# Kernel tuning notes

Measured on AMD Instinct MI355X. Metric: run time of the kernel, lower is better.

The kernel has to match this reference:

```python
import jax, jax.numpy as jnp
import numpy as np

B, N, NFEAT, NHID = 64, 133, 75, 128


def _uniform(key, shape, stdv):
    return jax.random.uniform(key, shape, minval=-stdv, maxval=stdv, dtype=jnp.float32)


def setup_inputs() -> dict:
    key = jax.random.key(0)
    ks = jax.random.split(key, 20)
    x = jax.random.normal(ks[0], (B, N, NFEAT), dtype=jnp.float32)
    mask = jax.random.uniform(ks[1], (B, N, N)) < 0.08
    adj = jnp.where(mask, jax.random.uniform(ks[2], (B, N, N), dtype=jnp.float32), 0.0)

    def lin(k, fin, fout):  # torch Linear default init ~ U(-1/sqrt(fin), 1/sqrt(fin))
        s = 1.0 / np.sqrt(fin)
        k1, k2 = jax.random.split(k)
        return _uniform(k1, (fin, fout), s), _uniform(k2, (fout,), s)

    def gc(k, fin, fout):  # GraphConvolution init ~ U(-1/sqrt(fout), 1/sqrt(fout))
        s = 1.0 / np.sqrt(fout)
        k1, k2 = jax.random.split(k)
        return _uniform(k1, (fin, fout), s), _uniform(k2, (fout,), s)

    emb_w, emb_b = lin(ks[3], NFEAT, 2 * NFEAT)
    gc1_w, gc1_b = gc(ks[4], 2 * NFEAT, 2 * NHID)
    gc2_w, gc2_b = gc(ks[5], 2 * NHID, NHID)
    gc3_w, gc3_b = gc(ks[6], NHID, NFEAT)
    gc4_w, gc4_b = gc(ks[7], NFEAT, 1)
    fc1_w, fc1_b = lin(ks[8], N - 1, 3)
    fin_w, fin_b = lin(ks[9], 4, 1)
    return dict(x=x, adj=adj, emb_w=emb_w, emb_b=emb_b,
                gc1_w=gc1_w, gc1_b=gc1_b, gc2_w=gc2_w, gc2_b=gc2_b,
                gc3_w=gc3_w, gc3_b=gc3_b, gc4_w=gc4_w, gc4_b=gc4_b,
                fc1_w=fc1_w, fc1_b=fc1_b, fin_w=fin_w, fin_b=fin_b)


def _gcn(x, adj, w, b):
    # output = adj @ (x @ W) + b   for each batch element
    return jnp.einsum('bij,bjf->bif', adj, x @ w) + b


def _graph_pooling(x, neibs):
    # per node i: max over features of neighbors j with neibs[b,i,j]; 0 if no neighbors
    masked = jnp.where(neibs[:, :, :, None], x[:, None, :, :], -jnp.inf)  # [B,N,N,F]
    pooled = jnp.max(masked, axis=2)                                       # [B,N,F]
    has_nb = jnp.any(neibs, axis=2)[:, :, None]                            # [B,N,1]
    return jnp.where(has_nb, pooled, 0.0)


def reference(x, adj, emb_w, emb_b, gc1_w, gc1_b, gc2_w, gc2_b,
              gc3_w, gc3_b, gc4_w, gc4_b, fc1_w, fc1_b, fin_w, fin_b):
    neibs = adj > 1e-5                                   # [B,N,N] bool
    h = jax.nn.relu(x @ emb_w + emb_b)                   # [B,N,2*nfeat]
    h = jax.nn.relu(_gcn(h, adj, gc1_w, gc1_b))          # [B,N,2*nhid]
    h = _graph_pooling(h, neibs)
    h = jax.nn.relu(_gcn(h, adj, gc2_w, gc2_b))          # [B,N,nhid]
    h = _graph_pooling(h, neibs)
    h = jax.nn.relu(_gcn(h, adj, gc3_w, gc3_b))          # [B,N,nfeat]
    h = _graph_pooling(h, neibs)
    h = jax.nn.relu(_gcn(h, adj, gc4_w, gc4_b))          # [B,N,1]
    h = h.reshape(h.shape[0], 1, -1)                     # [B,1,N]
    fst = h[:, :, :1]                                    # [B,1,1]
    rest = h[:, :, 1:]                                   # [B,1,N-1]
    # dropout is identity in eval mode
    rest = rest @ fc1_w + fc1_b                          # [B,1,3]
    out = jnp.concatenate((fst, rest), axis=2)           # [B,1,4]
    return jax.nn.sigmoid(out @ fin_w + fin_b)           # [B,1,1]
```

## Files before the change

kernel.cpp:

```cpp
#include <hip/hip_runtime.h>
#include <math.h>


#define NN 133
#define NPAIR 64
#define NW 16
#define ST 264

typedef float v4f __attribute__((ext_vector_type(4)));
typedef _Float16 f16x8 __attribute__((ext_vector_type(8)));
typedef _Float16 f16x4 __attribute__((ext_vector_type(4)));
typedef float f32x4 __attribute__((ext_vector_type(4)));

#define WP_EMB 0
#define WP_GC1 15360
#define WP_GC2 56320
#define WP_GC3 89088
#define WP_TOT 99328

struct Params {
    const float *x, *adj, *emb_w, *emb_b, *gc1_w, *gc1_b, *gc2_w, *gc2_b,
                *gc3_w, *gc3_b, *gc4_w, *gc4_b, *fc1_w, *fc1_b, *fin_w, *fin_b;
    const _Float16 *wp;
    float2 *gpairs;
    float *out;
};

__global__ __launch_bounds__(64)
void wpack_k(const float* __restrict__ emb_w, const float* __restrict__ gc1_w,
             const float* __restrict__ gc2_w, const float* __restrict__ gc3_w,
             _Float16* __restrict__ wp)
{
    const int t = blockIdx.x, lane = threadIdx.x;
    const float* W; int K, N, NKS, off, u;
    if (t < 30)       { W = emb_w; K = 75;  N = 150; NKS = 3; off = WP_EMB; u = t; }
    else if (t < 110) { W = gc1_w; K = 150; N = 256; NKS = 5; off = WP_GC1; u = t - 30; }
    else if (t < 174) { W = gc2_w; K = 256; N = 128; NKS = 8; off = WP_GC2; u = t - 110; }
    else              { W = gc3_w; K = 128; N = 75;  NKS = 4; off = WP_GC3; u = t - 174; }
    const int ct = u / NKS, ks = u % NKS;
    const int col = ct * 16 + (lane & 15);
    const int kb  = ks * 32 + (lane >> 4) * 8;
    f16x8 v;
#pragma unroll
    for (int j = 0; j < 8; ++j) {
        const int kk = kb + j;
        float w = W[(size_t)min(kk, K - 1) * N + min(col, N - 1)];
        if (kk >= K || col >= N) w = 0.f;
        v[j] = (_Float16)w;
    }
    *reinterpret_cast<f16x8*>(wp + (size_t)off + (size_t)u * 512 + lane * 8) = v;
}

__device__ __forceinline__ void prep_row_g(
    const float* __restrict__ ar, float2* __restrict__ pb,
    int2* __restrict__ cS, int r, int lane)
{
    const unsigned long long lt = (1ull << lane) - 1ull;
    int base0 = 0, base1 = 0;
#pragma unroll
    for (int s = 0; s < 3; ++s) {
        const int j = lane + 64 * s;
        const float a = (j < NN) ? ar[j] : 0.f;
        const bool f = a > 1e-5f;
        const bool g = (a > 0.f) && !f;
        const unsigned long long mf = __ballot(f);
        const unsigned long long mg = __ballot(g);
        if (f) pb[base0 + __popcll(mf & lt)] =
                   make_float2(a, __int_as_float(j));
        if (g) pb[(NPAIR - 1) - (base1 + __popcll(mg & lt))] =
                   make_float2(a, __int_as_float(j));
        base0 += __popcll(mf);
        base1 += __popcll(mg);
    }
    if (lane == 0) cS[r] = make_int2(base0, base1);
}

template<int KPAD, int N, int STN, int NTC, bool RB>
__device__ __forceinline__ void mfma_gemm(
    const _Float16* __restrict__ Af, const _Float16* __restrict__ Wp,
    const float* __restrict__ bias, _Float16* __restrict__ outl,
    int wave, int lane)
{
    const int lrow = lane & 15, lkb = lane >> 4;
    for (int t = wave; t < NTC * 9; t += NW) {
        const int ct = t % NTC, rt = t / NTC;
        const int col = ct * 16 + lrow;
        const _Float16* ap  = Af + (rt * 16 + lrow) * ST + lkb * 8;
        const _Float16* wpt = Wp + (size_t)(ct * (KPAD / 32)) * 512 + lane * 8;
        f32x4 acc = {0.f, 0.f, 0.f, 0.f};
#pragma unroll
        for (int ks = 0; ks < KPAD / 32; ++ks) {
            f16x8 a  = *reinterpret_cast<const f16x8*>(ap + ks * 32);
            f16x8 bf = *reinterpret_cast<const f16x8*>(wpt + ks * 512);
            acc = __builtin_amdgcn_mfma_f32_16x16x32_f16(a, bf, acc, 0, 0, 0);
        }
#pragma unroll
        for (int i = 0; i < 4; ++i) {
            const int row = rt * 16 + lkb * 4 + i;
            if (row < NN && col < STN) {
                float v = 0.f;
                if (col < N) {
                    v = acc[i];
                    if (RB) v = fmaxf(v + bias[col], 0.f);
                }
                outl[row * ST + col] = (_Float16)v;
            }
        }
    }
}

__device__ __forceinline__ void spmm4_lds(
    const _Float16* __restrict__ tb, const float* __restrict__ bias,
    const float2* __restrict__ pb, int2 cc,
    _Float16* __restrict__ yrow, int lane)
{
    const int c0 = 4 * lane;
    const float4* pq = reinterpret_cast<const float4*>(pb);
    float a0[4] = {}, a1[4] = {}, a2[4] = {}, a3[4] = {};
    int q = 0;
    for (; q + 4 <= cc.x; q += 4) {
        float4 p0 = pq[q >> 1], p1 = pq[(q >> 1) + 1];
        f16x4 r0 = *(const f16x4*)(tb + __float_as_int(p0.y) * ST + c0);
        f16x4 r1 = *(const f16x4*)(tb + __float_as_int(p0.w) * ST + c0);
        f16x4 r2 = *(const f16x4*)(tb + __float_as_int(p1.y) * ST + c0);
        f16x4 r3 = *(const f16x4*)(tb + __float_as_int(p1.w) * ST + c0);
#pragma unroll
        for (int u = 0; u < 4; ++u) {
            a0[u] = fmaf(p0.x, (float)r0[u], a0[u]);
            a1[u] = fmaf(p0.z, (float)r1[u], a1[u]);
            a2[u] = fmaf(p1.x, (float)r2[u], a2[u]);
            a3[u] = fmaf(p1.z, (float)r3[u], a3[u]);
        }
    }
    for (; q < cc.x; ++q) {
        float2 f = pb[q];
        f16x4 r = *(const f16x4*)(tb + __float_as_int(f.y) * ST + c0);
#pragma unroll
        for (int u = 0; u < 4; ++u) a0[u] = fmaf(f.x, (float)r[u], a0[u]);
    }
    for (int v = 0; v < cc.y; ++v) {
        float2 f = pb[(NPAIR - 1) - v];
        f16x4 r = *(const f16x4*)(tb + __float_as_int(f.y) * ST + c0);
#pragma unroll
        for (int u = 0; u < 4; ++u) a0[u] = fmaf(f.x, (float)r[u], a0[u]);
    }
    f16x4 o;
#pragma unroll
    for (int u = 0; u < 4; ++u) {
        float s = (a0[u] + a1[u]) + (a2[u] + a3[u]);
        o[u] = (_Float16)fmaxf(s + bias[c0 + u], 0.f);
    }
    *(f16x4*)(yrow + c0) = o;
}

__device__ __forceinline__ void pool4_lds(
    const _Float16* __restrict__ yb,
    const float2* __restrict__ pb, int cx,
    _Float16* __restrict__ prow, int lane)
{
    const int c0 = 4 * lane;
    const float4* pq = reinterpret_cast<const float4*>(pb);
    float m0[4] = {}, m1[4] = {}, m2[4] = {}, m3[4] = {};
    int q = 0;
    for (; q + 4 <= cx; q += 4) {
        float4 p0 = pq[q >> 1], p1 = pq[(q >> 1) + 1];
        f16x4 r0 = *(const f16x4*)(yb + __float_as_int(p0.y) * ST + c0);
        f16x4 r1 = *(const f16x4*)(yb + __float_as_int(p0.w) * ST + c0);
        f16x4 r2 = *(const f16x4*)(yb + __float_as_int(p1.y) * ST + c0);
        f16x4 r3 = *(const f16x4*)(yb + __float_as_int(p1.w) * ST + c0);
#pragma unroll
        for (int u = 0; u < 4; ++u) {
            m0[u] = fmaxf(m0[u], (float)r0[u]);
            m1[u] = fmaxf(m1[u], (float)r1[u]);
            m2[u] = fmaxf(m2[u], (float)r2[u]);
            m3[u] = fmaxf(m3[u], (float)r3[u]);
        }
    }
    for (; q < cx; ++q) {
        f16x4 r = *(const f16x4*)(yb + __float_as_int(pb[q].y) * ST + c0);
#pragma unroll
        for (int u = 0; u < 4; ++u) m0[u] = fmaxf(m0[u], (float)r[u]);
    }
    f16x4 o;
#pragma unroll
    for (int u = 0; u < 4; ++u)
        o[u] = (_Float16)fmaxf(fmaxf(m0[u], m1[u]), fmaxf(m2[u], m3[u]));
    *(f16x4*)(prow + c0) = o;
}

__device__ __forceinline__ void spmm2_lds(
    const _Float16* __restrict__ tb, const float* __restrict__ bias, int N,
    const float2* __restrict__ pb, int2 cc,
    _Float16* __restrict__ yrow, int lane)
{
    const int c0 = 2 * lane;
    const float4* pq = reinterpret_cast<const float4*>(pb);
    float a0[2] = {}, a1[2] = {}, a2[2] = {}, a3[2] = {};
    int q = 0;
    for (; q + 4 <= cc.x; q += 4) {
        float4 p0 = pq[q >> 1], p1 = pq[(q >> 1) + 1];
        f16x4 rr0 = *(const f16x4*)nullptr, rr1;
        (void)rr0; (void)rr1;
        const _Float16* t0 = tb + __float_as_int(p0.y) * ST + c0;
        const _Float16* t1 = tb + __float_as_int(p0.w) * ST + c0;
        const _Float16* t2 = tb + __float_as_int(p1.y) * ST + c0;
        const _Float16* t3 = tb + __float_as_int(p1.w) * ST + c0;
#pragma unroll
        for (int u = 0; u < 2; ++u) {
            a0[u] = fmaf(p0.x, (float)t0[u], a0[u]);
            a1[u] = fmaf(p0.z, (float)t1[u], a1[u]);
            a2[u] = fmaf(p1.x, (float)t2[u], a2[u]);
            a3[u] = fmaf(p1.z, (float)t3[u], a3[u]);
        }
    }
    for (; q < cc.x; ++q) {
        float2 f = pb[q];
        const _Float16* t0 = tb + __float_as_int(f.y) * ST + c0;
#pragma unroll
        for (int u = 0; u < 2; ++u) a0[u] = fmaf(f.x, (float)t0[u], a0[u]);
    }
    for (int v = 0; v < cc.y; ++v) {
        float2 f = pb[(NPAIR - 1) - v];
        const _Float16* t0 = tb + __float_as_int(f.y) * ST + c0;
#pragma unroll
        for (int u = 0; u < 2; ++u) a0[u] = fmaf(f.x, (float)t0[u], a0[u]);
    }
    float s0 = (a0[0] + a1[0]) + (a2[0] + a3[0]);
    float s1 = (a0[1] + a1[1]) + (a2[1] + a3[1]);
    s0 = fmaxf(s0 + bias[min(c0, N - 1)], 0.f);
    s1 = fmaxf(s1 + bias[min(c0 + 1, N - 1)], 0.f);
    if (c0 + 1 < N) {
        yrow[c0] = (_Float16)s0; yrow[c0 + 1] = (_Float16)s1;
    } else if (c0 < N) {
        yrow[c0] = (_Float16)s0;
    }
}

__device__ __forceinline__ void pool2_lds(
    const _Float16* __restrict__ yb, int N,
    const float2* __restrict__ pb, int cx,
    _Float16* __restrict__ prow, int lane)
{
    const int c0 = 2 * lane;
    const float4* pq = reinterpret_cast<const float4*>(pb);
    float m0[2] = {}, m1[2] = {}, m2[2] = {}, m3[2] = {};
    int q = 0;
    for (; q + 4 <= cx; q += 4) {
        float4 p0 = pq[q >> 1], p1 = pq[(q >> 1) + 1];
        const _Float16* t0 = yb + __float_as_int(p0.y) * ST + c0;
        const _Float16* t1 = yb + __float_as_int(p0.w) * ST + c0;
        const _Float16* t2 = yb + __float_as_int(p1.y) * ST + c0;
        const _Float16* t3 = yb + __float_as_int(p1.w) * ST + c0;
#pragma unroll
        for (int u = 0; u < 2; ++u) {
            m0[u] = fmaxf(m0[u], (float)t0[u]);
            m1[u] = fmaxf(m1[u], (float)t1[u]);
            m2[u] = fmaxf(m2[u], (float)t2[u]);
            m3[u] = fmaxf(m3[u], (float)t3[u]);
        }
    }
    for (; q < cx; ++q) {
        const _Float16* t0 = yb + __float_as_int(pb[q].y) * ST + c0;
#pragma unroll
        for (int u = 0; u < 2; ++u) m0[u] = fmaxf(m0[u], (float)t0[u]);
    }
    if (c0 + 1 < N) {
        prow[c0]     = (_Float16)fmaxf(fmaxf(m0[0], m1[0]), fmaxf(m2[0], m3[0]));
        prow[c0 + 1] = (_Float16)fmaxf(fmaxf(m0[1], m1[1]), fmaxf(m2[1], m3[1]));
    } else if (c0 < N) {
        prow[c0]     = (_Float16)fmaxf(fmaxf(m0[0], m1[0]), fmaxf(m2[0], m3[0]));
    }
}

__device__ __forceinline__ void t4_row_h(
    const _Float16* __restrict__ yb,
    const float2* __restrict__ pb, int cx,
    const float* __restrict__ gc4_w,
    float* __restrict__ t4S, int r, int lane)
{
    const float4* pq = reinterpret_cast<const float4*>(pb);
    const float gw0 = gc4_w[lane];
    const float gw1 = (lane < 11) ? gc4_w[64 + lane] : 0.f;
    const int c2 = 64 + min(lane, 10);

    float m0a = 0.f, m1a = 0.f, m0b = 0.f, m1b = 0.f;
    float m0c = 0.f, m1c = 0.f, m0d = 0.f, m1d = 0.f;
    int q = 0;
    for (; q + 4 <= cx; q += 4) {
        float4 pA = pq[q >> 1], pB = pq[(q >> 1) + 1];
        const _Float16* r0 = yb + __float_as_int(pA.y) * ST;
        const _Float16* r1 = yb + __float_as_int(pA.w) * ST;
        const _Float16* r2 = yb + __float_as_int(pB.y) * ST;
        const _Float16* r3 = yb + __float_as_int(pB.w) * ST;
        m0a = fmaxf(m0a, (float)r0[lane]); m1a = fmaxf(m1a, (float)r0[c2]);
        m0b = fmaxf(m0b, (float)r1[lane]); m1b = fmaxf(m1b, (float)r1[c2]);
        m0c = fmaxf(m0c, (float)r2[lane]); m1c = fmaxf(m1c, (float)r2[c2]);
        m0d = fmaxf(m0d, (float)r3[lane]); m1d = fmaxf(m1d, (float)r3[c2]);
    }
    for (; q < cx; ++q) {
        const _Float16* r0 = yb + __float_as_int(pb[q].y) * ST;
        m0a = fmaxf(m0a, (float)r0[lane]); m1a = fmaxf(m1a, (float)r0[c2]);
    }
    float m0 = fmaxf(fmaxf(m0a, m0b), fmaxf(m0c, m0d));
    float m1 = fmaxf(fmaxf(m1a, m1b), fmaxf(m1c, m1d));
    float v = m0 * gw0 + m1 * gw1;
#pragma unroll
    for (int off = 32; off; off >>= 1) v += __shfl_xor(v, off, 64);
    if (lane == 0) t4S[r] = v;
}

__global__ __launch_bounds__(1024, 1)
void graph_k(Params P)
{
    __shared__ __align__(16) _Float16 BUF[2][144 * ST];
    __shared__ int2  cS[NN];
    __shared__ float t4S[NN];
    __shared__ float y4S[NN];
    __shared__ float rS[3];

    const int b    = blockIdx.x;
    const int tid  = threadIdx.x;
    const int wave = tid >> 6, lane = tid & 63;

    _Float16* B0 = BUF[0];
    _Float16* B1 = BUF[1];
    float2* gp = P.gpairs + (size_t)b * NN * NPAIR;

    {
        v4f* z = reinterpret_cast<v4f*>(&BUF[0][0]);
        for (int i = tid; i < 2 * 144 * ST / 8; i += 1024)
            z[i] = v4f{0.f, 0.f, 0.f, 0.f};
    }
    __syncthreads();
    for (int i = tid; i < NN * 75; i += 1024) {
        int r = i / 75, c = i - r * 75;
        B1[r * ST + c] = (_Float16)P.x[(size_t)b * NN * 75 + i];
    }
    for (int r = wave; r < NN; r += NW)
        prep_row_g(P.adj + ((size_t)b * NN + r) * NN, gp + (size_t)r * NPAIR,
                   cS, r, lane);
    __syncthreads();
    mfma_gemm<96, 150, 150, 10, true>(B1, P.wp + WP_EMB, P.emb_b, B0, wave, lane);
    __syncthreads();
    mfma_gemm<160, 256, 256, 16, false>(B0, P.wp + WP_GC1, nullptr, B1, wave, lane);
    __syncthreads();
    for (int r = wave; r < NN; r += NW)
        spmm4_lds(B1, P.gc1_b, gp + (size_t)r * NPAIR, cS[r],
                  B0 + r * ST, lane);
    __syncthreads();
    for (int r = wave; r < NN; r += NW)
        pool4_lds(B0, gp + (size_t)r * NPAIR, cS[r].x, B1 + r * ST, lane);
    __syncthreads();
    mfma_gemm<256, 128, 128, 8, false>(B1, P.wp + WP_GC2, nullptr, B0, wave, lane);
    __syncthreads();
    for (int r = wave; r < NN; r += NW)
        spmm2_lds(B0, P.gc2_b, 128, gp + (size_t)r * NPAIR, cS[r],
                  B1 + r * ST, lane);
    __syncthreads();
    for (int r = wave; r < NN; r += NW)
        pool2_lds(B1, 128, gp + (size_t)r * NPAIR, cS[r].x, B0 + r * ST, lane);
    __syncthreads();
    mfma_gemm<128, 75, 76, 5, false>(B0, P.wp + WP_GC3, nullptr, B1, wave, lane);
    __syncthreads();
    for (int r = wave; r < NN; r += NW)
        spmm2_lds(B1, P.gc3_b, 75, gp + (size_t)r * NPAIR, cS[r],
                  B0 + r * ST, lane);
    __syncthreads();
    for (int r = wave; r < NN; r += NW)
        t4_row_h(B0, gp + (size_t)r * NPAIR, cS[r].x, P.gc4_w, t4S, r, lane);
    __syncthreads();
    if (tid < NN) {
        const float2* pb = gp + (size_t)tid * NPAIR;
        int2 c = cS[tid];
        float s = P.gc4_b[0];
        for (int q = 0; q < c.x; ++q) {
            float2 f = pb[q];
            s = fmaf(f.x, t4S[__float_as_int(f.y)], s);
        }
        for (int q = 0; q < c.y; ++q) {
            float2 f = pb[(NPAIR - 1) - q];
            s = fmaf(f.x, t4S[__float_as_int(f.y)], s);
        }
        y4S[tid] = fmaxf(s, 0.f);
    }
    __syncthreads();
    if (tid < 3) {
        float s = P.fc1_b[tid];
        for (int j = 0; j < 132; ++j)
            s = fmaf(y4S[1 + j], P.fc1_w[j * 3 + tid], s);
        rS[tid] = s;
    }
    __syncthreads();
    if (tid == 0) {
        float z = P.fin_b[0] + y4S[0] * P.fin_w[0] + rS[0] * P.fin_w[1]
                + rS[1] * P.fin_w[2] + rS[2] * P.fin_w[3];
        P.out[b] = 1.f / (1.f + expf(-z));
    }
}

extern "C" void kernel_launch(void* const* d_in, const int* in_sizes, int n_in,
                              void* d_out, int out_size, void* d_ws, size_t ws_size,
                              hipStream_t stream)
{
    _Float16* wp = (_Float16*)d_ws;
    float2* gpairs = (float2*)((char*)d_ws + (256 << 10));

    Params hp;
    hp.x     = (const float*)d_in[0];
    hp.adj   = (const float*)d_in[1];
    hp.emb_w = (const float*)d_in[2];
    hp.emb_b = (const float*)d_in[3];
    hp.gc1_w = (const float*)d_in[4];
    hp.gc1_b = (const float*)d_in[5];
    hp.gc2_w = (const float*)d_in[6];
    hp.gc2_b = (const float*)d_in[7];
    hp.gc3_w = (const float*)d_in[8];
    hp.gc3_b = (const float*)d_in[9];
    hp.gc4_w = (const float*)d_in[10];
    hp.gc4_b = (const float*)d_in[11];
    hp.fc1_w = (const float*)d_in[12];
    hp.fc1_b = (const float*)d_in[13];
    hp.fin_w = (const float*)d_in[14];
    hp.fin_b = (const float*)d_in[15];
    hp.wp = wp;
    hp.gpairs = gpairs;
    hp.out = (float*)d_out;

    hipLaunchKernelGGL(wpack_k, dim3(194), dim3(64), 0, stream,
                       hp.emb_w, hp.gc1_w, hp.gc2_w, hp.gc3_w, wp);
    hipLaunchKernelGGL(graph_k, dim3(64), dim3(1024), 0, stream, hp);
}
```

Baseline: 188.6 us.

## Replace gather-based sparse aggregation with dense fp16 MFMA adjacency matmul

The pack kernel now also converts each batch's adjacency into fp16 MFMA fragment layout. The graph kernel replaces the per-row gather SpMM loops with dense MFMA GEMMs against that packed adjacency, computing transposed (column-major) feature tiles so adj@T fits the MFMA operand layout. LDS is reorganised into two regions with tighter per-stage strides, and the pooling helpers are adjusted to match. The aim is to put aggregation on the matrix cores instead of scalar FMA gathers. The cost is dense work on a ~8%-sparse matrix, an extra 64 pack blocks that read all of adj, and fp16 rounding of adjacency values.

New measurement: 222.8 us, median of 2. 18.1% more time.

```diff
diff --git a/kernel.cpp b/kernel.cpp
--- a/kernel.cpp
+++ b/kernel.cpp
@@ -5,50 +5,73 @@
 #define NN 133
 #define NPAIR 64
 #define NW 16
-#define ST 264
+
+#define A0 0
+#define B0 37440
+#define SH_HALFS 80448
 
 typedef float v4f __attribute__((ext_vector_type(4)));
 typedef _Float16 f16x8 __attribute__((ext_vector_type(8)));
 typedef _Float16 f16x4 __attribute__((ext_vector_type(4)));
+typedef _Float16 f16x2 __attribute__((ext_vector_type(2)));
 typedef float f32x4 __attribute__((ext_vector_type(4)));
 
 #define WP_EMB 0
 #define WP_GC1 15360
 #define WP_GC2 56320
 #define WP_GC3 89088
-#define WP_TOT 99328
 
 struct Params {
     const float *x, *adj, *emb_w, *emb_b, *gc1_w, *gc1_b, *gc2_w, *gc2_b,
                 *gc3_w, *gc3_b, *gc4_w, *gc4_b, *fc1_w, *fc1_b, *fin_w, *fin_b;
     const _Float16 *wp;
+    const _Float16 *adjp;
     float2 *gpairs;
     float *out;
 };
 
 __global__ __launch_bounds__(64)
-void wpack_k(const float* __restrict__ emb_w, const float* __restrict__ gc1_w,
-             const float* __restrict__ gc2_w, const float* __restrict__ gc3_w,
-             _Float16* __restrict__ wp)
+void pack_k(const float* __restrict__ emb_w, const float* __restrict__ gc1_w,
+            const float* __restrict__ gc2_w, const float* __restrict__ gc3_w,
+            const float* __restrict__ adj,
+            _Float16* __restrict__ wp, _Float16* __restrict__ adjp)
 {
     const int t = blockIdx.x, lane = threadIdx.x;
-    const float* W; int K, N, NKS, off, u;
-    if (t < 30)       { W = emb_w; K = 75;  N = 150; NKS = 3; off = WP_EMB; u = t; }
-    else if (t < 110) { W = gc1_w; K = 150; N = 256; NKS = 5; off = WP_GC1; u = t - 30; }
-    else if (t < 174) { W = gc2_w; K = 256; N = 128; NKS = 8; off = WP_GC2; u = t - 110; }
-    else              { W = gc3_w; K = 128; N = 75;  NKS = 4; off = WP_GC3; u = t - 174; }
-    const int ct = u / NKS, ks = u % NKS;
-    const int col = ct * 16 + (lane & 15);
-    const int kb  = ks * 32 + (lane >> 4) * 8;
-    f16x8 v;
-#pragma unroll
-    for (int j = 0; j < 8; ++j) {
-        const int kk = kb + j;
-        float w = W[(size_t)min(kk, K - 1) * N + min(col, N - 1)];
-        if (kk >= K || col >= N) w = 0.f;
-        v[j] = (_Float16)w;
-    }
-    *reinterpret_cast<f16x8*>(wp + (size_t)off + (size_t)u * 512 + lane * 8) = v;
+    if (t < 194) {
+        const float* W; int K, N, NKS, off, u;
+        if (t < 30)       { W = emb_w; K = 75;  N = 150; NKS = 3; off = WP_EMB; u = t; }
+        else if (t < 110) { W = gc1_w; K = 150; N = 256; NKS = 5; off = WP_GC1; u = t - 30; }
+        else if (t < 174) { W = gc2_w; K = 256; N = 128; NKS = 8; off = WP_GC2; u = t - 110; }
+        else              { W = gc3_w; K = 128; N = 75;  NKS = 4; off = WP_GC3; u = t - 174; }
+        const int ct = u / NKS, ks = u % NKS;
+        const int col = ct * 16 + (lane & 15);
+        const int kb  = ks * 32 + (lane >> 4) * 8;
+        f16x8 v;
+#pragma unroll
+        for (int j = 0; j < 8; ++j) {
+            const int kk = kb + j;
+            float w = W[(size_t)min(kk, K - 1) * N + min(col, N - 1)];
+            if (kk >= K || col >= N) w = 0.f;
+            v[j] = (_Float16)w;
+        }
+        *reinterpret_cast<f16x8*>(wp + (size_t)off + (size_t)u * 512 + lane * 8) = v;
+    } else {
+        const int g = t - 194;
+        const float* ag = adj + (size_t)g * NN * NN;
+        for (int u = 0; u < 45; ++u) {
+            const int n  = (u / 5) * 16 + (lane & 15);
+            const int kb = (u % 5) * 32 + (lane >> 4) * 8;
+            f16x8 v;
+#pragma unroll
+            for (int j = 0; j < 8; ++j) {
+                const int kk = kb + j;
+                float w = (n < NN && kk < NN) ? ag[(size_t)n * NN + kk] : 0.f;
+                v[j] = (_Float16)w;
+            }
+            *reinterpret_cast<f16x8*>(
+                adjp + ((size_t)(g * 45 + u) * 64 + lane) * 8) = v;
+        }
+    }
 }
 
 __device__ __forceinline__ void prep_row_g(
@@ -75,85 +98,97 @@
     if (lane == 0) cS[r] = make_int2(base0, base1);
 }
 
-template<int KPAD, int N, int STN, int NTC, bool RB>
-__device__ __forceinline__ void mfma_gemm(
-    const _Float16* __restrict__ Af, const _Float16* __restrict__ Wp,
-    const float* __restrict__ bias, _Float16* __restrict__ outl,
+template<int MT, int NKS, int SSRC, int SDST, int N>
+__device__ __forceinline__ void gemm_rm(
+    const _Float16* __restrict__ wpA, const _Float16* __restrict__ src,
+    const float* __restrict__ bias, _Float16* __restrict__ dst,
     int wave, int lane)
 {
     const int lrow = lane & 15, lkb = lane >> 4;
-    for (int t = wave; t < NTC * 9; t += NW) {
-        const int ct = t % NTC, rt = t / NTC;
+    for (int t = wave; t < MT * 9; t += NW) {
+        const int mt = t % MT, nt = t / MT;
+        const _Float16* ap = wpA + (size_t)(mt * NKS) * 512 + lane * 8;
+        const _Float16* bp = src + (nt * 16 + lrow) * SSRC + lkb * 8;
+        f32x4 acc = {0.f, 0.f, 0.f, 0.f};
+#pragma unroll
+        for (int ks = 0; ks < NKS; ++ks) {
+            f16x8 a = *reinterpret_cast<const f16x8*>(ap + ks * 512);
+            f16x8 b = *reinterpret_cast<const f16x8*>(bp + ks * 32);
+            acc = __builtin_amdgcn_mfma_f32_16x16x32_f16(a, b, acc, 0, 0, 0);
+        }
+        const int row = nt * 16 + lrow;
+        const int c0  = mt * 16 + lkb * 4;
+        f16x4 o;
+#pragma unroll
+        for (int i = 0; i < 4; ++i) {
+            const int c = c0 + i;
+            float v = 0.f;
+            if (c < N) v = fmaxf(acc[i] + bias[c], 0.f);
+            o[i] = (_Float16)v;
+        }
+        *reinterpret_cast<f16x4*>(dst + row * SDST + c0) = o;
+    }
+}
+
+template<int CT, int NKS, int SSRC>
+__device__ __forceinline__ void gemm_cm(
+    const _Float16* __restrict__ src, const _Float16* __restrict__ wpB,
+    _Float16* __restrict__ t_cm, int wave, int lane)
+{
+    const int lrow = lane & 15, lkb = lane >> 4;
+    for (int t = wave; t < CT * 9; t += NW) {
+        const int ct = t % CT, rt = t / CT;
+        const _Float16* ap = src + (rt * 16 + lrow) * SSRC + lkb * 8;
+        const _Float16* bp = wpB + (size_t)(ct * NKS) * 512 + lane * 8;
+        f32x4 acc = {0.f, 0.f, 0.f, 0.f};
+#pragma unroll
+        for (int ks = 0; ks < NKS; ++ks) {
+            f16x8 a = *reinterpret_cast<const f16x8*>(ap + ks * 32);
+            f16x8 b = *reinterpret_cast<const f16x8*>(bp + ks * 512);
+            acc = __builtin_amdgcn_mfma_f32_16x16x32_f16(a, b, acc, 0, 0, 0);
+        }
         const int col = ct * 16 + lrow;
-        const _Float16* ap  = Af + (rt * 16 + lrow) * ST + lkb * 8;
-        const _Float16* wpt = Wp + (size_t)(ct * (KPAD / 32)) * 512 + lane * 8;
+        const int r0  = rt * 16 + lkb * 4;
+        f16x4 o;
+#pragma unroll
+        for (int i = 0; i < 4; ++i) o[i] = (_Float16)acc[i];
+        *reinterpret_cast<f16x4*>(t_cm + col * 168 + r0) = o;
+    }
+}
+
+template<int MT, int SDST, int N>
+__device__ __forceinline__ void spmm_mfma(
+    const _Float16* __restrict__ t_cm, const _Float16* __restrict__ adjB,
+    const float* __restrict__ bias, _Float16* __restrict__ y,
+    int wave, int lane)
+{
+    const int lrow = lane & 15, lkb = lane >> 4;
+    for (int t = wave; t < MT * 9; t += NW) {
+        const int mt = t % MT, nt = t / MT;
+        const _Float16* ap = t_cm + (mt * 16 + lrow) * 168 + lkb * 8;
+        const _Float16* bp = adjB + (size_t)(nt * 5) * 512 + lane * 8;
         f32x4 acc = {0.f, 0.f, 0.f, 0.f};
 #pragma unroll
-        for (int ks = 0; ks < KPAD / 32; ++ks) {
-            f16x8 a  = *reinterpret_cast<const f16x8*>(ap + ks * 32);
-            f16x8 bf = *reinterpret_cast<const f16x8*>(wpt + ks * 512);
-            acc = __builtin_amdgcn_mfma_f32_16x16x32_f16(a, bf, acc, 0, 0, 0);
-        }
+        for (int ks = 0; ks < 5; ++ks) {
+            f16x8 a = *reinterpret_cast<const f16x8*>(ap + ks * 32);
+            f16x8 b = *reinterpret_cast<const f16x8*>(bp + ks * 512);
+            acc = __builtin_amdgcn_mfma_f32_16x16x32_f16(a, b, acc, 0, 0, 0);
+        }
+        const int row = nt * 16 + lrow;
+        const int c0  = mt * 16 + lkb * 4;
+        f16x4 o;
 #pragma unroll
         for (int i = 0; i < 4; ++i) {
-            const int row = rt * 16 + lkb * 4 + i;
-            if (row < NN && col < STN) {
-                float v = 0.f;
-                if (col < N) {
-                    v = acc[i];
-                    if (RB) v = fmaxf(v + bias[col], 0.f);
-                }
-                outl[row * ST + col] = (_Float16)v;
-            }
-        }
-    }
-}
-
-__device__ __forceinline__ void spmm4_lds(
-    const _Float16* __restrict__ tb, const float* __restrict__ bias,
-    const float2* __restrict__ pb, int2 cc,
-    _Float16* __restrict__ yrow, int lane)
-{
-    const int c0 = 4 * lane;
-    const float4* pq = reinterpret_cast<const float4*>(pb);
-    float a0[4] = {}, a1[4] = {}, a2[4] = {}, a3[4] = {};
-    int q = 0;
-    for (; q + 4 <= cc.x; q += 4) {
-        float4 p0 = pq[q >> 1], p1 = pq[(q >> 1) + 1];
-        f16x4 r0 = *(const f16x4*)(tb + __float_as_int(p0.y) * ST + c0);
-        f16x4 r1 = *(const f16x4*)(tb + __float_as_int(p0.w) * ST + c0);
-        f16x4 r2 = *(const f16x4*)(tb + __float_as_int(p1.y) * ST + c0);
-        f16x4 r3 = *(const f16x4*)(tb + __float_as_int(p1.w) * ST + c0);
-#pragma unroll
-        for (int u = 0; u < 4; ++u) {
-            a0[u] = fmaf(p0.x, (float)r0[u], a0[u]);
-            a1[u] = fmaf(p0.z, (float)r1[u], a1[u]);
-            a2[u] = fmaf(p1.x, (float)r2[u], a2[u]);
-            a3[u] = fmaf(p1.z, (float)r3[u], a3[u]);
-        }
-    }
-    for (; q < cc.x; ++q) {
-        float2 f = pb[q];
-        f16x4 r = *(const f16x4*)(tb + __float_as_int(f.y) * ST + c0);
-#pragma unroll
-        for (int u = 0; u < 4; ++u) a0[u] = fmaf(f.x, (float)r[u], a0[u]);
-    }
-    for (int v = 0; v < cc.y; ++v) {
-        float2 f = pb[(NPAIR - 1) - v];
-        f16x4 r = *(const f16x4*)(tb + __float_as_int(f.y) * ST + c0);
-#pragma unroll
-        for (int u = 0; u < 4; ++u) a0[u] = fmaf(f.x, (float)r[u], a0[u]);
-    }
-    f16x4 o;
-#pragma unroll
-    for (int u = 0; u < 4; ++u) {
-        float s = (a0[u] + a1[u]) + (a2[u] + a3[u]);
-        o[u] = (_Float16)fmaxf(s + bias[c0 + u], 0.f);
-    }
-    *(f16x4*)(yrow + c0) = o;
-}
-
-__device__ __forceinline__ void pool4_lds(
+            const int c = c0 + i;
+            float v = 0.f;
+            if (c < N) v = fmaxf(acc[i] + bias[c], 0.f);
+            o[i] = (_Float16)v;
+        }
+        *reinterpret_cast<f16x4*>(y + row * SDST + c0) = o;
+    }
+}
+
+__device__ __forceinline__ void pool4(
     const _Float16* __restrict__ yb,
     const float2* __restrict__ pb, int cx,
     _Float16* __restrict__ prow, int lane)
@@ -164,10 +199,10 @@
     int q = 0;
     for (; q + 4 <= cx; q += 4) {
         float4 p0 = pq[q >> 1], p1 = pq[(q >> 1) + 1];
-        f16x4 r0 = *(const f16x4*)(yb + __float_as_int(p0.y) * ST + c0);
-        f16x4 r1 = *(const f16x4*)(yb + __float_as_int(p0.w) * ST + c0);
-        f16x4 r2 = *(const f16x4*)(yb + __float_as_int(p1.y) * ST + c0);
-        f16x4 r3 = *(const f16x4*)(yb + __float_as_int(p1.w) * ST + c0);
+        f16x4 r0 = *(const f16x4*)(yb + __float_as_int(p0.y) * 260 + c0);
+        f16x4 r1 = *(const f16x4*)(yb + __float_as_int(p0.w) * 260 + c0);
+        f16x4 r2 = *(const f16x4*)(yb + __float_as_int(p1.y) * 260 + c0);
+        f16x4 r3 = *(const f16x4*)(yb + __float_as_int(p1.w) * 260 + c0);
 #pragma unroll
         for (int u = 0; u < 4; ++u) {
             m0[u] = fmaxf(m0[u], (float)r0[u]);
@@ -177,7 +212,7 @@
         }
     }
     for (; q < cx; ++q) {
-        f16x4 r = *(const f16x4*)(yb + __float_as_int(pb[q].y) * ST + c0);
+        f16x4 r = *(const f16x4*)(yb + __float_as_int(pb[q].y) * 260 + c0);
 #pragma unroll
         for (int u = 0; u < 4; ++u) m0[u] = fmaxf(m0[u], (float)r[u]);
     }
@@ -188,118 +223,70 @@
     *(f16x4*)(prow + c0) = o;
 }
 
-__device__ __forceinline__ void spmm2_lds(
-    const _Float16* __restrict__ tb, const float* __restrict__ bias, int N,
-    const float2* __restrict__ pb, int2 cc,
-    _Float16* __restrict__ yrow, int lane)
-{
-    const int c0 = 2 * lane;
-    const float4* pq = reinterpret_cast<const float4*>(pb);
-    float a0[2] = {}, a1[2] = {}, a2[2] = {}, a3[2] = {};
-    int q = 0;
-    for (; q + 4 <= cc.x; q += 4) {
-        float4 p0 = pq[q >> 1], p1 = pq[(q >> 1) + 1];
-        f16x4 rr0 = *(const f16x4*)nullptr, rr1;
-        (void)rr0; (void)rr1;
-        const _Float16* t0 = tb + __float_as_int(p0.y) * ST + c0;
-        const _Float16* t1 = tb + __float_as_int(p0.w) * ST + c0;
-        const _Float16* t2 = tb + __float_as_int(p1.y) * ST + c0;
-        const _Float16* t3 = tb + __float_as_int(p1.w) * ST + c0;
-#pragma unroll
-        for (int u = 0; u < 2; ++u) {
-            a0[u] = fmaf(p0.x, (float)t0[u], a0[u]);
-            a1[u] = fmaf(p0.z, (float)t1[u], a1[u]);
-            a2[u] = fmaf(p1.x, (float)t2[u], a2[u]);
-            a3[u] = fmaf(p1.z, (float)t3[u], a3[u]);
-        }
-    }
-    for (; q < cc.x; ++q) {
-        float2 f = pb[q];
-        const _Float16* t0 = tb + __float_as_int(f.y) * ST + c0;
-#pragma unroll
-        for (int u = 0; u < 2; ++u) a0[u] = fmaf(f.x, (float)t0[u], a0[u]);
-    }
-    for (int v = 0; v < cc.y; ++v) {
-        float2 f = pb[(NPAIR - 1) - v];
-        const _Float16* t0 = tb + __float_as_int(f.y) * ST + c0;
-#pragma unroll
-        for (int u = 0; u < 2; ++u) a0[u] = fmaf(f.x, (float)t0[u], a0[u]);
-    }
-    float s0 = (a0[0] + a1[0]) + (a2[0] + a3[0]);
-    float s1 = (a0[1] + a1[1]) + (a2[1] + a3[1]);
-    s0 = fmaxf(s0 + bias[min(c0, N - 1)], 0.f);
-    s1 = fmaxf(s1 + bias[min(c0 + 1, N - 1)], 0.f);
-    if (c0 + 1 < N) {
-        yrow[c0] = (_Float16)s0; yrow[c0 + 1] = (_Float16)s1;
-    } else if (c0 < N) {
-        yrow[c0] = (_Float16)s0;
-    }
-}
-
-__device__ __forceinline__ void pool2_lds(
-    const _Float16* __restrict__ yb, int N,
+__device__ __forceinline__ void pool2(
+    const _Float16* __restrict__ yb,
     const float2* __restrict__ pb, int cx,
     _Float16* __restrict__ prow, int lane)
 {
     const int c0 = 2 * lane;
+    if (c0 >= 128) return;
     const float4* pq = reinterpret_cast<const float4*>(pb);
     float m0[2] = {}, m1[2] = {}, m2[2] = {}, m3[2] = {};
     int q = 0;
     for (; q + 4 <= cx; q += 4) {
         float4 p0 = pq[q >> 1], p1 = pq[(q >> 1) + 1];
-        const _Float16* t0 = yb + __float_as_int(p0.y) * ST + c0;
-        const _Float16* t1 = yb + __float_as_int(p0.w) * ST + c0;
-        const _Float16* t2 = yb + __float_as_int(p1.y) * ST + c0;
-        const _Float16* t3 = yb + __float_as_int(p1.w) * ST + c0;
+        f16x2 r0 = *(const f16x2*)(yb + __float_as_int(p0.y) * 136 + c0);
+        f16x2 r1 = *(const f16x2*)(yb + __float_as_int(p0.w) * 136 + c0);
+        f16x2 r2 = *(const f16x2*)(yb + __float_as_int(p1.y) * 136 + c0);
+        f16x2 r3 = *(const f16x2*)(yb + __float_as_int(p1.w) * 136 + c0);
 #pragma unroll
         for (int u = 0; u < 2; ++u) {
-            m0[u] = fmaxf(m0[u], (float)t0[u]);
-            m1[u] = fmaxf(m1[u], (float)t1[u]);
-            m2[u] = fmaxf(m2[u], (float)t2[u]);
-            m3[u] = fmaxf(m3[u], (float)t3[u]);
+            m0[u] = fmaxf(m0[u], (float)r0[u]);
+            m1[u] = fmaxf(m1[u], (float)r1[u]);
+            m2[u] = fmaxf(m2[u], (float)r2[u]);
+            m3[u] = fmaxf(m3[u], (float)r3[u]);
         }
     }
     for (; q < cx; ++q) {
-        const _Float16* t0 = yb + __float_as_int(pb[q].y) * ST + c0;
-#pragma unroll
-        for (int u = 0; u < 2; ++u) m0[u] = fmaxf(m0[u], (float)t0[u]);
-    }
-    if (c0 + 1 < N) {
-        prow[c0]     = (_Float16)fmaxf(fmaxf(m0[0], m1[0]), fmaxf(m2[0], m3[0]));
-        prow[c0 + 1] = (_Float16)fmaxf(fmaxf(m0[1], m1[1]), fmaxf(m2[1], m3[1]));
-    } else if (c0 < N) {
-        prow[c0]     = (_Float16)fmaxf(fmaxf(m0[0], m1[0]), fmaxf(m2[0], m3[0]));
-    }
-}
-
-__device__ __forceinline__ void t4_row_h(
+        f16x2 r = *(const f16x2*)(yb + __float_as_int(pb[q].y) * 136 + c0);
+#pragma unroll
+        for (int u = 0; u < 2; ++u) m0[u] = fmaxf(m0[u], (float)r[u]);
+    }
+    f16x2 o;
+#pragma unroll
+    for (int u = 0; u < 2; ++u)
+        o[u] = (_Float16)fmaxf(fmaxf(m0[u], m1[u]), fmaxf(m2[u], m3[u]));
+    *(f16x2*)(prow + c0) = o;
+}
+
+__device__ __forceinline__ void t4_row(
     const _Float16* __restrict__ yb,
     const float2* __restrict__ pb, int cx,
     const float* __restrict__ gc4_w,
     float* __restrict__ t4S, int r, int lane)
 {
+    const int c0 = 2 * lane;
+    const int sc = min(c0, 78);
+    const float gw0 = (c0 < 75) ? gc4_w[c0] : 0.f;
+    const float gw1 = (c0 + 1 < 75) ? gc4_w[c0 + 1] : 0.f;
     const float4* pq = reinterpret_cast<const float4*>(pb);
-    const float gw0 = gc4_w[lane];
-    const float gw1 = (lane < 11) ? gc4_w[64 + lane] : 0.f;
-    const int c2 = 64 + min(lane, 10);
-
     float m0a = 0.f, m1a = 0.f, m0b = 0.f, m1b = 0.f;
     float m0c = 0.f, m1c = 0.f, m0d = 0.f, m1d = 0.f;
     int q = 0;
     for (; q + 4 <= cx; q += 4) {
         float4 pA = pq[q >> 1], pB = pq[(q >> 1) + 1];
-        const _Float16* r0 = yb + __float_as_int(pA.y) * ST;
-        const _Float16* r1 = yb + __float_as_int(pA.w) * ST;
-        const _Float16* r2 = yb + __float_as_int(pB.y) * ST;
-        const _Float16* r3 = yb + __float_as_int(pB.w) * ST;
-        m0a = fmaxf(m0a, (float)r0[lane]); m1a = fmaxf(m1a, (float)r0[c2]);
-        m0b = fmaxf(m0b, (float)r1[lane]); m1b = fmaxf(m1b, (float)r1[c2]);
-        m0c = fmaxf(m0c, (float)r2[lane]); m1c = fmaxf(m1c, (float)r2[c2]);
-        m0d = fmaxf(m0d, (float)r3[lane]); m1d = fmaxf(m1d, (float)r3[c2]);
+        f16x2 r0 = *(const f16x2*)(yb + __float_as_int(pA.y) * 80 + sc);
+        f16x2 r1 = *(const f16x2*)(yb + __float_as_int(pA.w) * 80 + sc);
+        f16x2 r2 = *(const f16x2*)(yb + __float_as_int(pB.y) * 80 + sc);
+        f16x2 r3 = *(const f16x2*)(yb + __float_as_int(pB.w) * 80 + sc);
+        m0a = fmaxf(m0a, (float)r0[0]); m1a = fmaxf(m1a, (float)r0[1]);
+        m0b = fmaxf(m0b, (float)r1[0]); m1b = fmaxf(m1b, (float)r1[1]);
+        m0c = fmaxf(m0c, (float)r2[0]); m1c = fmaxf(m1c, (float)r2[1]);
+        m0d = fmaxf(m0d, (float)r3[0]); m1d = fmaxf(m1d, (float)r3[1]);
     }
     for (; q < cx; ++q) {
-        const _Float16* r0 = yb + __float_as_int(pb[q].y) * ST;
-        m0a = fmaxf(m0a, (float)r0[lane]); m1a = fmaxf(m1a, (float)r0[c2]);
+        f16x2 r = *(const f16x2*)(yb + __float_as_int(pb[q].y) * 80 + sc);
+        m0a = fmaxf(m0a, (float)r[0]); m1a = fmaxf(m1a, (float)r[1]);
     }
     float m0 = fmaxf(fmaxf(m0a, m0b), fmaxf(m0c, m0d));
     float m1 = fmaxf(fmaxf(m1a, m1b), fmaxf(m1c, m1d));
@@ -312,7 +299,7 @@
 __global__ __launch_bounds__(1024, 1)
 void graph_k(Params P)
 {
-    __shared__ __align__(16) _Float16 BUF[2][144 * ST];
+    __shared__ __align__(16) _Float16 SH[SH_HALFS];
     __shared__ int2  cS[NN];
     __shared__ float t4S[NN];
     __shared__ float y4S[NN];
@@ -322,52 +309,49 @@
     const int tid  = threadIdx.x;
     const int wave = tid >> 6, lane = tid & 63;
 
-    _Float16* B0 = BUF[0];
-    _Float16* B1 = BUF[1];
     float2* gp = P.gpairs + (size_t)b * NN * NPAIR;
+    const _Float16* adjB = P.adjp + (size_t)b * 45 * 512;
 
     {
-        v4f* z = reinterpret_cast<v4f*>(&BUF[0][0]);
-        for (int i = tid; i < 2 * 144 * ST / 8; i += 1024)
+        v4f* z = reinterpret_cast<v4f*>(&SH[0]);
+        for (int i = tid; i < SH_HALFS / 8; i += 1024)
             z[i] = v4f{0.f, 0.f, 0.f, 0.f};
-    }
-    __syncthreads();
-    for (int i = tid; i < NN * 75; i += 1024) {
-        int r = i / 75, c = i - r * 75;
-        B1[r * ST + c] = (_Float16)P.x[(size_t)b * NN * 75 + i];
     }
     for (int r = wave; r < NN; r += NW)
         prep_row_g(P.adj + ((size_t)b * NN + r) * NN, gp + (size_t)r * NPAIR,
                    cS, r, lane);
     __syncthreads();
-    mfma_gemm<96, 150, 150, 10, true>(B1, P.wp + WP_EMB, P.emb_b, B0, wave, lane);
-    __syncthreads();
-    mfma_gemm<160, 256, 256, 16, false>(B0, P.wp + WP_GC1, nullptr, B1, wave, lane);
+    for (int i = tid; i < NN * 75; i += 1024) {
+        int r = i / 75, c = i - r * 75;
+        SH[B0 + r * 104 + c] = (_Float16)P.x[(size_t)b * NN * 75 + i];
+    }
+    __syncthreads();
+    gemm_rm<10, 3, 104, 168, 150>(P.wp + WP_EMB, SH + B0, P.emb_b,
+                                  SH + A0, wave, lane);
+    __syncthreads();
+    gemm_cm<16, 5, 168>(SH + A0, P.wp + WP_GC1, SH + B0, wave, lane);
+    __syncthreads();
+    spmm_mfma<16, 260, 256>(SH + B0, adjB, P.gc1_b, SH + A0, wave, lane);
     __syncthreads();
     for (int r = wave; r < NN; r += NW)
-        spmm4_lds(B1, P.gc1_b, gp + (size_t)r * NPAIR, cS[r],
-                  B0 + r * ST, lane);
+        pool4(SH + A0, gp + (size_t)r * NPAIR, cS[r].x,
+              SH + B0 + r * 264, lane);
+    __syncthreads();
+    gemm_cm<8, 8, 264>(SH + B0, P.wp + WP_GC2, SH + A0, wave, lane);
+    __syncthreads();
+    spmm_mfma<8, 136, 128>(SH + A0, adjB, P.gc2_b, SH + B0, wave, lane);
     __syncthreads();
     for (int r = wave; r < NN; r += NW)
-        pool4_lds(B0, gp + (size_t)r * NPAIR, cS[r].x, B1 + r * ST, lane);
-    __syncthreads();
-    mfma_gemm<256, 128, 128, 8, false>(B1, P.wp + WP_GC2, nullptr, B0, wave, lane);
+        pool2(SH + B0, gp + (size_t)r * NPAIR, cS[r].x,
+              SH + A0 + r * 136, lane);
+    __syncthreads();
+    gemm_cm<5, 4, 136>(SH + A0, P.wp + WP_GC3, SH + B0, wave, lane);
+    __syncthreads();
+    spmm_mfma<5, 80, 75>(SH + B0, adjB, P.gc3_b, SH + A0, wave, lane);
     __syncthreads();
     for (int r = wave; r < NN; r += NW)
-        spmm2_lds(B0, P.gc2_b, 128, gp + (size_t)r * NPAIR, cS[r],
-                  B1 + r * ST, lane);
-    __syncthreads();
-    for (int r = wave; r < NN; r += NW)
-        pool2_lds(B1, 128, gp + (size_t)r * NPAIR, cS[r].x, B0 + r * ST, lane);
-    __syncthreads();
-    mfma_gemm<128, 75, 76, 5, false>(B0, P.wp + WP_GC3, nullptr, B1, wave, lane);
-    __syncthreads();
-    for (int r = wave; r < NN; r += NW)
-        spmm2_lds(B1, P.gc3_b, 75, gp + (size_t)r * NPAIR, cS[r],
-                  B0 + r * ST, lane);
-    __syncthreads();
-    for (int r = wave; r < NN; r += NW)
-        t4_row_h(B0, gp + (size_t)r * NPAIR, cS[r].x, P.gc4_w, t4S, r, lane);
+        t4_row(SH + A0, gp + (size_t)r * NPAIR, cS[r].x, P.gc4_w,
+               t4S, r, lane);
     __syncthreads();
     if (tid < NN) {
         const float2* pb = gp + (size_t)tid * NPAIR;
@@ -402,8 +386,9 @@
                               void* d_out, int out_size, void* d_ws, size_t ws_size,
                               hipStream_t stream)
 {
-    _Float16* wp = (_Float16*)d_ws;
-    float2* gpairs = (float2*)((char*)d_ws + (256 << 10));
+    _Float16* wp    = (_Float16*)d_ws;
+    _Float16* adjp  = (_Float16*)((char*)d_ws + (256 << 10));
+    float2*   gpairs = (float2*)((char*)d_ws + (256 << 10) + (3 << 20));
 
     Params hp;
     hp.x     = (const float*)d_in[0];
@@ -423,10 +408,12 @@
     hp.fin_w = (const float*)d_in[14];
     hp.fin_b = (const float*)d_in[15];
     hp.wp = wp;
+    hp.adjp = adjp;
     hp.gpairs = gpairs;
     hp.out = (float*)d_out;
 
-    hipLaunchKernelGGL(wpack_k, dim3(194), dim3(64), 0, stream,
-                       hp.emb_w, hp.gc1_w, hp.gc2_w, hp.gc3_w, wp);
+    hipLaunchKernelGGL(pack_k, dim3(258), dim3(64), 0, stream,
+                       hp.emb_w, hp.gc1_w, hp.gc2_w, hp.gc3_w, hp.adj,
+                       (_Float16*)wp, (_Float16*)adjp);
     hipLaunchKernelGGL(graph_k, dim3(64), dim3(1024), 0, stream, hp);
 }
```
